# Kernel tuning notes

Measured on AMD Instinct MI355X. Metric: run time of the kernel, lower is better.

Reference implementation:

```python
import jax, jax.numpy as jnp
import numpy as np

N_SRC, N_DST, MAX_NEIGH, H = 65536, 8192, 32, 128


def setup_inputs() -> dict:
    key = jax.random.key(0)
    ks = jax.random.split(key, 16)
    inp = {
        'x': jax.random.randint(ks[0], (N_SRC, 2), 0, 1000, dtype=jnp.int64)
             if jax.config.jax_enable_x64 else jax.random.randint(ks[0], (N_SRC, 2), 0, 1000, dtype=jnp.int32),
        'neigh_sim': jax.random.randint(ks[1], (N_DST, MAX_NEIGH), 0, N_SRC, dtype=jnp.int32),
        'neigh_cor': jax.random.randint(ks[2], (N_DST, MAX_NEIGH), 0, N_SRC, dtype=jnp.int32),
        'emb0_sim': jax.random.normal(ks[3], (1000, 32), jnp.float32) * 0.1,
        'emb1_sim': jax.random.normal(ks[4], (100000, 96), jnp.float32) * 0.1,
        'emb0_cor': jax.random.normal(ks[5], (1000, 32), jnp.float32) * 0.1,
        'emb1_cor': jax.random.normal(ks[6], (100000, 96), jnp.float32) * 0.1,
        'W_in_sim': jax.random.normal(ks[7], (H, H), jnp.float32) * 0.05,
        'b_in_sim': jnp.zeros((H,), jnp.float32),
        'W_in_cor': jax.random.normal(ks[8], (H, H), jnp.float32) * 0.05,
        'b_in_cor': jnp.zeros((H,), jnp.float32),
        'W_out_sim': jax.random.normal(ks[9], (H, H), jnp.float32) * 0.05,
        'b_out_sim': jnp.zeros((H,), jnp.float32),
        'W_out_cor': jax.random.normal(ks[10], (H, H), jnp.float32) * 0.05,
        'b_out_cor': jnp.zeros((H,), jnp.float32),
        'W_sim2cor': jax.random.normal(ks[11], (H, H), jnp.float32) * 0.05,
        'W_cor2sim': jax.random.normal(ks[12], (H, H), jnp.float32) * 0.05,
    }
    return inp


def _coattention_pool(D, Q):
    # D, Q: [N, m, H]
    n, m, h = Q.shape
    L = jnp.einsum('nmh,nkh->nmk', D, Q)           # [N, m, m]
    AC = jax.nn.softmax(L, axis=-1)
    AS = jax.nn.softmax(jnp.swapaxes(L, 1, 2), axis=-1)
    CQ = jnp.einsum('nmk,nkh->nmh', AC, Q)          # [N, m, H]
    CD = jnp.einsum('nkm,nmh->nkh', AS, jnp.concatenate([D, CQ], axis=-1))  # [N, m, 2H]
    out = jnp.concatenate([Q, CD], axis=-1)         # [N, m, 3H]
    # AvgPool1d(kernel=3, stride=3) over channel dim, then mean over neighbors
    pooled = out.reshape(n, m, h, 3).mean(axis=-1)  # consecutive triples
    return pooled.mean(axis=1)                       # [N, H]


def _mode_forward(x, neigh_sim, neigh_cor, emb0, emb1, W_in, b_in, W_out, b_out, mode):
    feat = jnp.concatenate([emb0[x[:, 0]], emb1[x[:, 1]]], axis=-1)  # [N_src, 128]
    feat = feat @ W_in + b_in                                        # [N_src, H]
    h_self = feat[: neigh_sim.shape[0]]
    nf_sim = feat[neigh_sim]  # [N_dst, m, H]
    nf_cor = feat[neigh_cor]
    if mode == 'cor':
        D, Q = nf_sim, nf_cor
    else:
        D, Q = nf_cor, nf_sim
    rst = h_self + _coattention_pool(D, Q)
    return rst @ W_out + b_out


def reference(x, neigh_sim, neigh_cor, emb0_sim, emb1_sim, emb0_cor, emb1_cor,
              W_in_sim, b_in_sim, W_in_cor, b_in_cor,
              W_out_sim, b_out_sim, W_out_cor, b_out_cor,
              W_sim2cor, W_cor2sim):
    sim = _mode_forward(x, neigh_sim, neigh_cor, emb0_sim, emb1_sim,
                        W_in_sim, b_in_sim, W_out_sim, b_out_sim, 'sim')
    cor = _mode_forward(x, neigh_sim, neigh_cor, emb0_cor, emb1_cor,
                        W_in_cor, b_in_cor, W_out_cor, b_out_cor, 'cor')
    a1, a2, b2 = 0.5, 0.33, 0.33
    z1sim = (1 - a1) * sim + a1 * (cor @ W_cor2sim)
    z1cor = (1 - a1) * cor + a1 * (sim @ W_sim2cor)
    z2sim = (1 - a2 - b2) * sim + a2 * (cor @ W_cor2sim) + b2 * (z1cor @ W_cor2sim)
    z2cor = (1 - a2 - b2) * cor + a2 * (sim @ W_sim2cor) + b2 * (z1sim @ W_sim2cor)
    return z2sim, z2cor
```

## Files before the change

kernel.cpp:

```cpp
#include <hip/hip_runtime.h>
#include <hip/hip_bf16.h>

#define NSRC 65536
#define NDST 8192
#define H 128

#define C_SELF 0.34f
#define C_CROSS 0.495f
#define C_DBL  0.165f

typedef float f32x16 __attribute__((ext_vector_type(16)));
typedef short bf16x8 __attribute__((ext_vector_type(8)));

static __device__ __forceinline__ float b2f(unsigned short u) {
  union { unsigned int i; float f; } v; v.i = ((unsigned int)u) << 16; return v.f;
}
static __device__ __forceinline__ unsigned short f2b(float f) {
  union { float f; unsigned int i; } v; v.f = f;
  unsigned int x = v.i;
  return (unsigned short)((x + 0x7fffu + ((x >> 16) & 1u)) >> 16);
}
static __device__ __forceinline__ void load4bf(const unsigned short* p, float* d) {
  ushort4 u = *(const ushort4*)p;
  d[0] = b2f(u.x); d[1] = b2f(u.y); d[2] = b2f(u.z); d[3] = b2f(u.w);
}
static __device__ __forceinline__ float fp8_manual(unsigned int b) {
  const unsigned e = (b >> 3) & 15u, m = b & 7u;
  union { unsigned i; float f; } v; v.i = ((e + 120u) << 23) | (m << 20);
  float f = (e == 0u) ? (float)m * 1.953125e-3f : v.f;
  return (b & 0x80u) ? -f : f;
}
static __device__ __forceinline__ void fp8x4_to_f32(int w, float* out) {
#if __has_builtin(__builtin_amdgcn_cvt_f32_fp8)
  out[0] = __builtin_amdgcn_cvt_f32_fp8(w, 0);
  out[1] = __builtin_amdgcn_cvt_f32_fp8(w, 1);
  out[2] = __builtin_amdgcn_cvt_f32_fp8(w, 2);
  out[3] = __builtin_amdgcn_cvt_f32_fp8(w, 3);
#else
  out[0] = fp8_manual((unsigned)w & 0xFFu);
  out[1] = fp8_manual(((unsigned)w >> 8) & 0xFFu);
  out[2] = fp8_manual(((unsigned)w >> 16) & 0xFFu);
  out[3] = fp8_manual(((unsigned)w >> 24) & 0xFFu);
#endif
}

template <int CTRL>
static __device__ __forceinline__ float dpp_mov(float x) {
  return __int_as_float(__builtin_amdgcn_update_dpp(
      0, __float_as_int(x), CTRL, 0xF, 0xF, true));
}
static __device__ __forceinline__ float dpp_sum32_tail(float x) {
  x += dpp_mov<0x111>(x);
  x += dpp_mov<0x112>(x);
  x += dpp_mov<0x114>(x);
  x += dpp_mov<0x118>(x);
  x += dpp_mov<0x142>(x);
  return x;
}
static __device__ __forceinline__ float allred32_sum(float x) {
  x += dpp_mov<0xB1>(x);
  x += dpp_mov<0x4E>(x);
  x += dpp_mov<0x124>(x);
  x += dpp_mov<0x128>(x);
  x += __int_as_float(__builtin_amdgcn_ds_swizzle(__float_as_int(x), 0x401F));
  return x;
}

static __device__ __forceinline__ void load4any(const void* base, size_t idx, int f32flag, float* d) {
  if (f32flag) {
    float4 v = *(const float4*)((const float*)base + idx);
    d[0] = v.x; d[1] = v.y; d[2] = v.z; d[3] = v.w;
  } else {
    load4bf((const unsigned short*)base + idx, d);
  }
}
static __device__ __forceinline__ float load1any(const void* base, size_t idx, int f32flag) {
  return f32flag ? ((const float*)base)[idx] : b2f(((const unsigned short*)base)[idx]);
}

__global__ void detect(const unsigned short* __restrict__ W, const int* __restrict__ x,
                       int* __restrict__ flags) {
  const int l = threadIdx.x;
  int bad = 0;
#pragma unroll
  for (int i = l; i < 128; i += 64) {
    unsigned short u = W[i];
    if (u != 0) {
      int e = (u >> 7) & 0xFF;
      if (e < 90 || e > 128) bad++;
    }
  }
  int nz = (l < 16) ? (x[2 * l + 1] != 0 ? 1 : 0) : 0;
#pragma unroll
  for (int d = 1; d < 64; d <<= 1) {
    bad += __shfl_xor(bad, d);
    nz  += __shfl_xor(nz, d);
  }
  if (l == 0) {
    flags[0] = (bad > 8) ? 1 : 0;
    flags[1] = (nz == 0) ? 1 : 0;
  }
}

__global__ __launch_bounds__(128) void wprep(
    const void* __restrict__ Wsim, const void* __restrict__ Wcor,
    const int* __restrict__ flags,
    unsigned short* __restrict__ WTsim, unsigned short* __restrict__ WTcor)
{
  const int wf = flags[0];
  const int n = blockIdx.x & 127;
  const void* W = (blockIdx.x & 128) ? Wcor : Wsim;
  unsigned short* WT = (blockIdx.x & 128) ? WTcor : WTsim;
  const int k = threadIdx.x;
  WT[n * 128 + k] = f2b(load1any(W, k * 128 + n, wf));
}

__global__ __launch_bounds__(256) void featgemm_mfma(
    const int* __restrict__ x,
    const void* __restrict__ emb0,
    const void* __restrict__ emb1,
    const unsigned short* __restrict__ WT,
    const void* __restrict__ bvec,
    const int* __restrict__ flags,
    unsigned char* __restrict__ feat8,
    unsigned short* __restrict__ feat16)
{
  const int wf  = flags[0];
  const int x64 = flags[1];
  const int t = threadIdx.x;
  const int w = t >> 6, l = t & 63, lane = l & 31, half = l >> 5;
  const int rbase = blockIdx.x * 128 + w * 32;
  const int r = rbase + lane;

  int x0, x1;
  if (x64) { x0 = x[r * 4]; x1 = x[r * 4 + 2]; }
  else     { x0 = x[r * 2]; x1 = x[r * 2 + 1]; }

  bf16x8 afrag[8];
#pragma unroll
  for (int s = 0; s < 8; ++s) {
    float tmp[8];
    if (s < 2) {
      const size_t base = (size_t)x0 * 32 + s * 16 + half * 8;
      load4any(emb0, base, wf, tmp);
      load4any(emb0, base + 4, wf, tmp + 4);
    } else {
      const size_t base = (size_t)x1 * 96 + (s * 16 - 32) + half * 8;
      load4any(emb1, base, wf, tmp);
      load4any(emb1, base + 4, wf, tmp + 4);
    }
    union { bf16x8 v; unsigned short u[8]; } cv;
#pragma unroll
    for (int j = 0; j < 8; ++j) cv.u[j] = f2b(tmp[j]);
    afrag[s] = cv.v;
  }

  const bool do16 = (rbase < NDST);
#pragma unroll
  for (int strip = 0; strip < 4; ++strip) {
    const int n = strip * 32 + lane;
    const unsigned short* wtrow = WT + (size_t)n * 128 + half * 8;
    f32x16 acc = {0,0,0,0,0,0,0,0,0,0,0,0,0,0,0,0};
#pragma unroll
    for (int s = 0; s < 8; ++s) {
      bf16x8 bfrag = *(const bf16x8*)(wtrow + s * 16);
      acc = __builtin_amdgcn_mfma_f32_32x32x16_bf16(afrag[s], bfrag, acc, 0, 0, 0);
    }
    const float bias_n = load1any(bvec, n, wf);
#pragma unroll
    for (int i = 0; i < 16; ++i) {
      const int m = (i & 3) + 8 * (i >> 2) + 4 * half;
      const int row = rbase + m;
      const float val = acc[i] + bias_n;
      const int p8 = __builtin_amdgcn_cvt_pk_fp8_f32(val, val, 0, false);
      feat8[(size_t)row * H + n] = (unsigned char)(p8 & 0xFF);
      if (do16) feat16[(size_t)row * H + n] = f2b(val);
    }
  }
}

__global__ __launch_bounds__(256) void coatt_mfma(
    const unsigned char* __restrict__ feat8,
    const unsigned short* __restrict__ feat16,
    const int* __restrict__ idxD,
    const int* __restrict__ idxQ,
    unsigned short* __restrict__ rst)
{
  __shared__ float gbuf[4][416];
  const int t = threadIdx.x;
  const int w = t >> 6;
  const int l = t & 63;
  const int r = l & 31;
  const int half = l >> 5;
  const int n = blockIdx.x * 4 + w;

  float* g   = gbuf[w];
  float* svb = gbuf[w] + 384;

  const int gD = idxD[n * 32 + r];
  const int gQ = idxQ[n * 32 + r];
  const unsigned char* drow = feat8 + (size_t)gD * H + half * 8;
  const unsigned char* qrow = feat8 + (size_t)gQ * H + half * 8;

  long dfrag[8], qfrag[8];
#pragma unroll
  for (int s = 0; s < 8; ++s) {
    dfrag[s] = *(const long*)(drow + s * 16);
    qfrag[s] = *(const long*)(qrow + s * 16);
  }

  f32x16 acc = {0,0,0,0,0,0,0,0,0,0,0,0,0,0,0,0};
#pragma unroll
  for (int s = 0; s < 8; ++s)
    acc = __builtin_amdgcn_mfma_f32_32x32x16_fp8_fp8(dfrag[s], qfrag[s], acc, 0, 0, 0);

  float ex[16], rrcp[16];
#pragma unroll
  for (int i = 0; i < 16; ++i) ex[i] = __expf(acc[i]);
#pragma unroll
  for (int i = 0; i < 16; ++i) rrcp[i] = 1.0f / allred32_sum(ex[i]);
  float csum = 0.f;
#pragma unroll
  for (int i = 0; i < 16; ++i) csum += ex[i];
  csum += __shfl_xor(csum, 32);
  const float crcp = 1.0f / csum;

  float svt[16];
#pragma unroll
  for (int i = 0; i < 16; ++i) svt[i] = dpp_sum32_tail(ex[i] * crcp);
  if (r == 31) {
    *(float4*)(svb + 4 * half)      = make_float4(svt[0],  svt[1],  svt[2],  svt[3]);
    *(float4*)(svb + 8 + 4 * half)  = make_float4(svt[4],  svt[5],  svt[6],  svt[7]);
    *(float4*)(svb + 16 + 4 * half) = make_float4(svt[8],  svt[9],  svt[10], svt[11]);
    *(float4*)(svb + 24 + 4 * half) = make_float4(svt[12], svt[13], svt[14], svt[15]);
  }
  float sv16[16];
#pragma unroll
  for (int q = 0; q < 4; ++q) {
    float4 v = *(const float4*)(svb + q * 8 + 4 * half);
    sv16[q * 4] = v.x; sv16[q * 4 + 1] = v.y; sv16[q * 4 + 2] = v.z; sv16[q * 4 + 3] = v.w;
  }
  const float svl = svb[r];
  float tvp = 0.f;
#pragma unroll
  for (int i = 0; i < 16; ++i) tvp += sv16[i] * ex[i] * rrcp[i];
  const float tv = tvp + __shfl_xor(tvp, 32);

#pragma unroll
  for (int s = 0; s < 8; ++s) {
    int2 dw = *(int2*)&dfrag[s];
    int2 qw = *(int2*)&qfrag[s];
    float dv[8], qv[8];
    fp8x4_to_f32(dw.x, dv); fp8x4_to_f32(dw.y, dv + 4);
    fp8x4_to_f32(qw.x, qv); fp8x4_to_f32(qw.y, qv + 4);
    float uq[8], vd[8], wq[8];
#pragma unroll
    for (int j = 0; j < 8; ++j) {
      uq[j] = dpp_sum32_tail(qv[j]);
      vd[j] = dpp_sum32_tail(svl * dv[j]);
      wq[j] = dpp_sum32_tail(tv * qv[j]);
    }
    if (r == 31) {
      const int hb = s * 16 + half * 8;
      *(float4*)(g + hb)           = make_float4(uq[0], uq[1], uq[2], uq[3]);
      *(float4*)(g + hb + 4)       = make_float4(uq[4], uq[5], uq[6], uq[7]);
      *(float4*)(g + 128 + hb)     = make_float4(vd[0], vd[1], vd[2], vd[3]);
      *(float4*)(g + 128 + hb + 4) = make_float4(vd[4], vd[5], vd[6], vd[7]);
      *(float4*)(g + 256 + hb)     = make_float4(wq[0], wq[1], wq[2], wq[3]);
      *(float4*)(g + 256 + hb + 4) = make_float4(wq[4], wq[5], wq[6], wq[7]);
    }
  }

#pragma unroll
  for (int rep = 0; rep < 2; ++rep) {
    const int hp = l + rep * 64;
    const float p = (g[3 * hp] + g[3 * hp + 1] + g[3 * hp + 2]) * (1.0f / 96.0f);
    const float hs = b2f(feat16[(size_t)n * H + hp]);
    rst[(size_t)n * H + hp] = f2b(hs + p);
  }
}

__global__ __launch_bounds__(128) void smallmm1(
    const void* __restrict__ Wos, const void* __restrict__ Woc,
    const void* __restrict__ Wsc, const void* __restrict__ Wcs,
    const void* __restrict__ bs, const void* __restrict__ bc,
    const int* __restrict__ flags,
    float* __restrict__ P1, float* __restrict__ P2,
    unsigned short* __restrict__ P1T, unsigned short* __restrict__ P2T,
    float* __restrict__ p1, float* __restrict__ p2)
{
  const int wf = flags[0];
  const int bid = blockIdx.x, c = threadIdx.x;
  if (bid < 128) {
    const int r = bid; float acc = 0.f;
    for (int k = 0; k < 128; ++k) acc += load1any(Wos, r * 128 + k, wf) * load1any(Wsc, k * 128 + c, wf);
    P1[r * 128 + c] = acc;
    P1T[c * 128 + r] = f2b(acc);
  } else if (bid < 256) {
    const int r = bid - 128; float acc = 0.f;
    for (int k = 0; k < 128; ++k) acc += load1any(Woc, r * 128 + k, wf) * load1any(Wcs, k * 128 + c, wf);
    P2[r * 128 + c] = acc;
    P2T[c * 128 + r] = f2b(acc);
  } else if (bid == 256) {
    float acc = 0.f;
    for (int k = 0; k < 128; ++k) acc += load1any(bs, k, wf) * load1any(Wsc, k * 128 + c, wf);
    p1[c] = acc;
  } else {
    float acc = 0.f;
    for (int k = 0; k < 128; ++k) acc += load1any(bc, k, wf) * load1any(Wcs, k * 128 + c, wf);
    p2[c] = acc;
  }
}

__global__ __launch_bounds__(128) void smallmm2(
    const void* __restrict__ Wos, const void* __restrict__ Woc,
    const void* __restrict__ Wsc, const void* __restrict__ Wcs,
    const void* __restrict__ bs, const void* __restrict__ bc,
    const int* __restrict__ flags,
    const float* __restrict__ P1, const float* __restrict__ P2,
    const float* __restrict__ p1, const float* __restrict__ p2,
    unsigned short* __restrict__ MssT, unsigned short* __restrict__ MccT,
    float* __restrict__ bsim, float* __restrict__ bcor)
{
  const int wf = flags[0];
  const int bid = blockIdx.x, c = threadIdx.x;
  if (bid < 128) {
    const int r = bid; float acc = 0.f;
    for (int k = 0; k < 128; ++k) acc += P1[r * 128 + k] * load1any(Wcs, k * 128 + c, wf);
    MssT[c * 128 + r] = f2b(C_SELF * load1any(Wos, r * 128 + c, wf) + C_DBL * acc);
  } else if (bid < 256) {
    const int r = bid - 128; float acc = 0.f;
    for (int k = 0; k < 128; ++k) acc += P2[r * 128 + k] * load1any(Wsc, k * 128 + c, wf);
    MccT[c * 128 + r] = f2b(C_SELF * load1any(Woc, r * 128 + c, wf) + C_DBL * acc);
  } else if (bid == 256) {
    float acc = 0.f;
    for (int k = 0; k < 128; ++k) acc += p1[k] * load1any(Wcs, k * 128 + c, wf);
    bsim[c] = C_SELF * load1any(bs, c, wf) + C_CROSS * p2[c] + C_DBL * acc;
  } else {
    float acc = 0.f;
    for (int k = 0; k < 128; ++k) acc += p2[k] * load1any(Wsc, k * 128 + c, wf);
    bcor[c] = C_SELF * load1any(bc, c, wf) + C_CROSS * p1[c] + C_DBL * acc;
  }
}

__global__ __launch_bounds__(256) void finalmm_mfma(
    const unsigned short* __restrict__ Rs, const unsigned short* __restrict__ Rc,
    const unsigned short* __restrict__ MssT, const unsigned short* __restrict__ MccT,
    const unsigned short* __restrict__ P1T, const unsigned short* __restrict__ P2T,
    const float* __restrict__ bsim, const float* __restrict__ bcor,
    float* __restrict__ outp)
{
  const int t = threadIdx.x;
  const int w = t >> 6, l = t & 63, lane = l & 31, half = l >> 5;
  const int rbase = blockIdx.x * 32;
  const int arow = rbase + lane;
  const int n = w * 32 + lane;

  const unsigned short* rsrow = Rs + (size_t)arow * H + half * 8;
  const unsigned short* rcrow = Rc + (size_t)arow * H + half * 8;
  bf16x8 aS[8], aC[8];
#pragma unroll
  for (int s = 0; s < 8; ++s) {
    aS[s] = *(const bf16x8*)(rsrow + s * 16);
    aC[s] = *(const bf16x8*)(rcrow + s * 16);
  }

  const unsigned short* bMss = MssT + (size_t)n * 128 + half * 8;
  const unsigned short* bMcc = MccT + (size_t)n * 128 + half * 8;
  const unsigned short* bP1  = P1T  + (size_t)n * 128 + half * 8;
  const unsigned short* bP2  = P2T  + (size_t)n * 128 + half * 8;

  f32x16 a1 = {0,0,0,0,0,0,0,0,0,0,0,0,0,0,0,0};
  f32x16 a2 = a1, a3 = a1, a4 = a1;
#pragma unroll
  for (int s = 0; s < 8; ++s) {
    bf16x8 b1 = *(const bf16x8*)(bMss + s * 16);
    bf16x8 b2 = *(const bf16x8*)(bP2  + s * 16);
    bf16x8 b3 = *(const bf16x8*)(bMcc + s * 16);
    bf16x8 b4 = *(const bf16x8*)(bP1  + s * 16);
    a1 = __builtin_amdgcn_mfma_f32_32x32x16_bf16(aS[s], b1, a1, 0, 0, 0);
    a2 = __builtin_amdgcn_mfma_f32_32x32x16_bf16(aC[s], b2, a2, 0, 0, 0);
    a3 = __builtin_amdgcn_mfma_f32_32x32x16_bf16(aC[s], b3, a3, 0, 0, 0);
    a4 = __builtin_amdgcn_mfma_f32_32x32x16_bf16(aS[s], b4, a4, 0, 0, 0);
  }

  const float bsv = bsim[n], bcv = bcor[n];
#pragma unroll
  for (int i = 0; i < 16; ++i) {
    const int m = (i & 3) + 8 * (i >> 2) + 4 * half;
    const int row = rbase + m;
    outp[(size_t)row * H + n] = a1[i] + C_CROSS * a2[i] + bsv;
    outp[(size_t)NDST * H + (size_t)row * H + n] = a3[i] + C_CROSS * a4[i] + bcv;
  }
}

extern "C" void kernel_launch(void* const* d_in, const int* in_sizes, int n_in,
                              void* d_out, int out_size, void* d_ws, size_t ws_size,
                              hipStream_t stream) {
  const int* x    = (const int*)d_in[0];
  const int* nsim = (const int*)d_in[1];
  const int* ncor = (const int*)d_in[2];
  const void* emb0_sim = d_in[3];
  const void* emb1_sim = d_in[4];
  const void* emb0_cor = d_in[5];
  const void* emb1_cor = d_in[6];
  const void* W_in_sim  = d_in[7];
  const void* b_in_sim  = d_in[8];
  const void* W_in_cor  = d_in[9];
  const void* b_in_cor  = d_in[10];
  const void* W_out_sim = d_in[11];
  const void* b_out_sim = d_in[12];
  const void* W_out_cor = d_in[13];
  const void* b_out_cor = d_in[14];
  const void* W_sim2cor = d_in[15];
  const void* W_cor2sim = d_in[16];

  float* fbase = (float*)d_ws;
  float* P1  = fbase;
  float* P2  = P1 + H * H;
  float* p1v = P2 + H * H;
  float* p2v = p1v + H;
  float* bsimv = p2v + H;
  float* bcorv = bsimv + H;
  int* flags = (int*)(bcorv + H);
  unsigned short* feat16_sim = (unsigned short*)(flags + 4);
  unsigned short* feat16_cor = feat16_sim + (size_t)NDST * H;
  unsigned short* rst_sim    = feat16_cor + (size_t)NDST * H;
  unsigned short* rst_cor    = rst_sim + (size_t)NDST * H;
  unsigned char* feat8_sim = (unsigned char*)(rst_cor + (size_t)NDST * H);
  unsigned char* feat8_cor = feat8_sim + (size_t)NSRC * H;
  unsigned short* WT_sim = (unsigned short*)(feat8_cor + (size_t)NSRC * H);
  unsigned short* WT_cor = WT_sim + H * H;
  unsigned short* P1T  = WT_cor + H * H;
  unsigned short* P2T  = P1T + H * H;
  unsigned short* MssT = P2T + H * H;
  unsigned short* MccT = MssT + H * H;

  detect<<<1, 64, 0, stream>>>((const unsigned short*)W_in_sim, x, flags);
  wprep<<<256, 128, 0, stream>>>(W_in_sim, W_in_cor, flags, WT_sim, WT_cor);
  smallmm1<<<258, 128, 0, stream>>>(W_out_sim, W_out_cor, W_sim2cor, W_cor2sim,
                                    b_out_sim, b_out_cor, flags, P1, P2, P1T, P2T, p1v, p2v);
  smallmm2<<<258, 128, 0, stream>>>(W_out_sim, W_out_cor, W_sim2cor, W_cor2sim,
                                    b_out_sim, b_out_cor, flags, P1, P2, p1v, p2v,
                                    MssT, MccT, bsimv, bcorv);
  featgemm_mfma<<<NSRC / 128, 256, 0, stream>>>(x, emb0_sim, emb1_sim, WT_sim, b_in_sim,
                                                flags, feat8_sim, feat16_sim);
  featgemm_mfma<<<NSRC / 128, 256, 0, stream>>>(x, emb0_cor, emb1_cor, WT_cor, b_in_cor,
                                                flags, feat8_cor, feat16_cor);
  coatt_mfma<<<NDST / 4, 256, 0, stream>>>(feat8_sim, feat16_sim, ncor, nsim, rst_sim);
  coatt_mfma<<<NDST / 4, 256, 0, stream>>>(feat8_cor, feat16_cor, nsim, ncor, rst_cor);
  finalmm_mfma<<<NDST / 32, 256, 0, stream>>>(rst_sim, rst_cor, MssT, MccT, P1T, P2T,
                                              bsimv, bcorv, (float*)d_out);
}
```

Baseline: 271.2 us.

## Transpose fp8 fragments via identity MFMA instead of DPP column reductions

```diff
diff --git a/kernel.cpp b/kernel.cpp
--- a/kernel.cpp
+++ b/kernel.cpp
@@ -23,25 +23,6 @@
 static __device__ __forceinline__ void load4bf(const unsigned short* p, float* d) {
   ushort4 u = *(const ushort4*)p;
   d[0] = b2f(u.x); d[1] = b2f(u.y); d[2] = b2f(u.z); d[3] = b2f(u.w);
-}
-static __device__ __forceinline__ float fp8_manual(unsigned int b) {
-  const unsigned e = (b >> 3) & 15u, m = b & 7u;
-  union { unsigned i; float f; } v; v.i = ((e + 120u) << 23) | (m << 20);
-  float f = (e == 0u) ? (float)m * 1.953125e-3f : v.f;
-  return (b & 0x80u) ? -f : f;
-}
-static __device__ __forceinline__ void fp8x4_to_f32(int w, float* out) {
-#if __has_builtin(__builtin_amdgcn_cvt_f32_fp8)
-  out[0] = __builtin_amdgcn_cvt_f32_fp8(w, 0);
-  out[1] = __builtin_amdgcn_cvt_f32_fp8(w, 1);
-  out[2] = __builtin_amdgcn_cvt_f32_fp8(w, 2);
-  out[3] = __builtin_amdgcn_cvt_f32_fp8(w, 3);
-#else
-  out[0] = fp8_manual((unsigned)w & 0xFFu);
-  out[1] = fp8_manual(((unsigned)w >> 8) & 0xFFu);
-  out[2] = fp8_manual(((unsigned)w >> 16) & 0xFFu);
-  out[3] = fp8_manual(((unsigned)w >> 24) & 0xFFu);
-#endif
 }
 
 template <int CTRL>
@@ -186,7 +167,7 @@
     const int* __restrict__ idxQ,
     unsigned short* __restrict__ rst)
 {
-  __shared__ float gbuf[4][416];
+  __shared__ float gbuf[4][448];
   const int t = threadIdx.x;
   const int w = t >> 6;
   const int l = t & 63;
@@ -196,6 +177,7 @@
 
   float* g   = gbuf[w];
   float* svb = gbuf[w] + 384;
+  float* tvb = gbuf[w] + 416;
 
   const int gD = idxD[n * 32 + r];
   const int gQ = idxQ[n * 32 + r];
@@ -240,34 +222,42 @@
     float4 v = *(const float4*)(svb + q * 8 + 4 * half);
     sv16[q * 4] = v.x; sv16[q * 4 + 1] = v.y; sv16[q * 4 + 2] = v.z; sv16[q * 4 + 3] = v.w;
   }
-  const float svl = svb[r];
   float tvp = 0.f;
 #pragma unroll
   for (int i = 0; i < 16; ++i) tvp += sv16[i] * ex[i] * rrcp[i];
   const float tv = tvp + __shfl_xor(tvp, 32);
 
+  if (l < 32) tvb[l] = tv;
+  float tv16[16];
+#pragma unroll
+  for (int q = 0; q < 4; ++q) {
+    float4 vv = *(const float4*)(tvb + q * 8 + 4 * half);
+    tv16[q * 4] = vv.x; tv16[q * 4 + 1] = vv.y; tv16[q * 4 + 2] = vv.z; tv16[q * 4 + 3] = vv.w;
+  }
+
+  const int bpos = (l & 15) - half * 8;
+  const long b_ident = (bpos >= 0 && bpos < 8) ? (0x38L << (8 * bpos)) : 0L;
+  const f32x16 zf = {0,0,0,0,0,0,0,0,0,0,0,0,0,0,0,0};
+
 #pragma unroll
   for (int s = 0; s < 8; ++s) {
-    int2 dw = *(int2*)&dfrag[s];
-    int2 qw = *(int2*)&qfrag[s];
-    float dv[8], qv[8];
-    fp8x4_to_f32(dw.x, dv); fp8x4_to_f32(dw.y, dv + 4);
-    fp8x4_to_f32(qw.x, qv); fp8x4_to_f32(qw.y, qv + 4);
-    float uq[8], vd[8], wq[8];
-#pragma unroll
-    for (int j = 0; j < 8; ++j) {
-      uq[j] = dpp_sum32_tail(qv[j]);
-      vd[j] = dpp_sum32_tail(svl * dv[j]);
-      wq[j] = dpp_sum32_tail(tv * qv[j]);
-    }
-    if (r == 31) {
-      const int hb = s * 16 + half * 8;
-      *(float4*)(g + hb)           = make_float4(uq[0], uq[1], uq[2], uq[3]);
-      *(float4*)(g + hb + 4)       = make_float4(uq[4], uq[5], uq[6], uq[7]);
-      *(float4*)(g + 128 + hb)     = make_float4(vd[0], vd[1], vd[2], vd[3]);
-      *(float4*)(g + 128 + hb + 4) = make_float4(vd[4], vd[5], vd[6], vd[7]);
-      *(float4*)(g + 256 + hb)     = make_float4(wq[0], wq[1], wq[2], wq[3]);
-      *(float4*)(g + 256 + hb + 4) = make_float4(wq[4], wq[5], wq[6], wq[7]);
+    f32x16 td = __builtin_amdgcn_mfma_f32_32x32x16_fp8_fp8(dfrag[s], b_ident, zf, 0, 0, 0);
+    f32x16 tq = __builtin_amdgcn_mfma_f32_32x32x16_fp8_fp8(qfrag[s], b_ident, zf, 0, 0, 0);
+    float su = 0.f, sw = 0.f, sv_ = 0.f;
+#pragma unroll
+    for (int i = 0; i < 16; ++i) {
+      su  += tq[i];
+      sw  += tv16[i] * tq[i];
+      sv_ += sv16[i] * td[i];
+    }
+    su  += __shfl_xor(su, 32);
+    sw  += __shfl_xor(sw, 32);
+    sv_ += __shfl_xor(sv_, 32);
+    if (l < 16) {
+      const int c = s * 16 + l;
+      g[c]       = su;
+      g[128 + c] = sv_;
+      g[256 + c] = sw;
     }
   }
 
```

Measured after the change: 248.2 us. 1.09x faster.
